# Performance work log

Hardware: AMD Instinct MI355X
Metric: run time of the kernel (lower is better)

The kernel has to match this reference:

```python
import jax, jax.numpy as jnp
import numpy as np

B, S, D, H = 4, 1024, 1024, 16
HD = D // H  # head dim = 64


def setup_inputs() -> dict:
    key = jax.random.key(0)
    ks = jax.random.split(key, 12)
    inv = 1.0 / np.sqrt(D)
    inp = {
        "q": jax.random.normal(ks[0], (B, S, D), jnp.float32),
        "k": jax.random.normal(ks[1], (B, S, D), jnp.float32),
        "v": jax.random.normal(ks[2], (B, S, D), jnp.float32),
        # additive-style mask: 1 where attention is disallowed (causal)
        "mask": jnp.triu(jnp.ones((S, S), jnp.float32), k=1)[None, None, :, :],
        "Wq": jax.random.normal(ks[3], (D, D), jnp.float32) * inv,
        "bq": jnp.zeros((D,), jnp.float32),
        "Wk": jax.random.normal(ks[4], (D, D), jnp.float32) * inv,
        "bk": jnp.zeros((D,), jnp.float32),
        "Wv": jax.random.normal(ks[5], (D, D), jnp.float32) * inv,
        "bv": jnp.zeros((D,), jnp.float32),
        "Wo": jax.random.normal(ks[6], (D, D), jnp.float32) * inv,
        "bo": jnp.zeros((D,), jnp.float32),
    }
    return inp


def _split_heads(x):
    # [b, s, (h d)] -> [b, h, s, d]
    b, s, _ = x.shape
    return x.reshape(b, s, H, HD).transpose(0, 2, 1, 3)


def reference(q, k, v, mask, Wq, bq, Wk, bk, Wv, bv, Wo, bo):
    query = _split_heads(q @ Wq + bq)   # [b,h,s,d]
    key = _split_heads(k @ Wk + bk)
    value = _split_heads(v @ Wv + bv)

    scores = jnp.einsum("bhqd,bhkd->bhqk", query, key) / np.sqrt(HD)
    scores = scores + mask * (-1e12)
    attention_weights = jax.nn.softmax(scores, axis=-1)  # [b,h,s,s]
    attn = jnp.einsum("bhqk,bhkd->bhqd", attention_weights, value)

    # dropout is identity in eval mode
    attn = attn.transpose(0, 2, 1, 3).reshape(q.shape[0], q.shape[1], D)
    out = attn @ Wo + bo
    return out, attention_weights
```

## Files before the change

### kernel.cpp

```cpp
#include <hip/hip_runtime.h>
#include <hip/hip_bf16.h>

#define B_ 4
#define S_ 1024
#define D_ 1024
#define H_ 16
#define HD_ 64
#define M_ (B_*S_)
#define NT_ (S_/64)

typedef __attribute__((ext_vector_type(8))) short bf16x8;
typedef __attribute__((ext_vector_type(8))) unsigned short u16x8;
typedef __attribute__((ext_vector_type(4))) float f32x4;

typedef __attribute__((address_space(1))) const unsigned int g_uint;
typedef __attribute__((address_space(3))) unsigned int l_uint;

__device__ __forceinline__ unsigned short f2bf(float f) {
  unsigned int x = __builtin_bit_cast(unsigned int, f);
  unsigned int r = (x + 0x7fffu + ((x >> 16) & 1u)) >> 16;
  return (unsigned short)r;
}
__device__ __forceinline__ float bf2f(unsigned short u) {
  unsigned int x = ((unsigned int)u) << 16;
  return __builtin_bit_cast(float, x);
}
__device__ __forceinline__ unsigned int cvtpk(float lo, float hi) {
  unsigned int r;
  asm("v_cvt_pk_bf16_f32 %0, %1, %2" : "=v"(r) : "v"(lo), "v"(hi));
  return r;
}
__device__ __forceinline__ void load_lds16(const ushort* g, ushort* l) {
  __builtin_amdgcn_global_load_lds((g_uint*)g, (l_uint*)l, 16, 0, 0);
}

__global__ void prep(const float* __restrict__ q, const float* __restrict__ k,
                     const float* __restrict__ v,
                     const float* __restrict__ Wq, const float* __restrict__ Wk,
                     const float* __restrict__ Wv, const float* __restrict__ Wo,
                     ushort* __restrict__ qo, ushort* __restrict__ ko, ushort* __restrict__ vo,
                     ushort* __restrict__ WqT, ushort* __restrict__ WkT,
                     ushort* __restrict__ WvT, ushort* __restrict__ WoT) {
  __shared__ float tile[32][33];
  int z = blockIdx.y;
  if (z < 3) {
    const float* s; ushort* d;
    switch (z) {
      case 0: s = q; d = qo; break;
      case 1: s = k; d = ko; break;
      default: s = v; d = vo; break;
    }
    int n4 = (M_ * D_) / 4;
    for (int i = blockIdx.x * blockDim.x + threadIdx.x; i < n4; i += gridDim.x * blockDim.x) {
      float4 x = reinterpret_cast<const float4*>(s)[i];
      ushort4 o;
      o.x = f2bf(x.x); o.y = f2bf(x.y); o.z = f2bf(x.z); o.w = f2bf(x.w);
      reinterpret_cast<ushort4*>(d)[i] = o;
    }
  } else {
    if (blockIdx.x >= 1024) return;
    const float* W; ushort* WT;
    switch (z - 3) {
      case 0: W = Wq; WT = WqT; break;
      case 1: W = Wk; WT = WkT; break;
      case 2: W = Wv; WT = WvT; break;
      default: W = Wo; WT = WoT; break;
    }
    int tx = threadIdx.x & 31, ty = threadIdx.x >> 5;
    int bx = (blockIdx.x & 31) * 32, by = (blockIdx.x >> 5) * 32;
    for (int r = 0; r < 32; r += 8)
      tile[ty + r][tx] = W[(size_t)(by + ty + r) * D_ + bx + tx];
    __syncthreads();
    for (int r = 0; r < 32; r += 8)
      WT[(size_t)(bx + ty + r) * D_ + by + tx] = f2bf(tile[tx][ty + r]);
  }
}

template <int BF16OUT, int BM, int BN>
__device__ __forceinline__ void gemm_body(const ushort* __restrict__ A,
                                          const ushort* __restrict__ Bt,
                                          const float* __restrict__ bias,
                                          void* __restrict__ Cp,
                                          int bm, int bn, int N, int K) {
  __shared__ ushort Al[BM * 64];
  __shared__ ushort Bl[BN * 64];
  constexpr int MF = BM / 32;
  constexpr int NF = BN / 32;
  const int tid = threadIdx.x;
  const int wave = tid >> 6, lane = tid & 63;
  const int r0 = lane & 15, kq = lane >> 4;
  const int wr = wave >> 1, wc = wave & 1;
  const int sl = lane >> 3;
  const int sc8 = ((lane & 7) ^ sl) * 8;
  f32x4 zero = {0.f, 0.f, 0.f, 0.f};
  f32x4 acc[MF][NF];
#pragma unroll
  for (int m = 0; m < MF; ++m)
#pragma unroll
    for (int n = 0; n < NF; ++n) acc[m][n] = zero;

  for (int kt = 0; kt < K; kt += 64) {
    __syncthreads();
#pragma unroll
    for (int i = 0; i < MF; ++i) {
      int c = wave * MF + i;
      load_lds16(A + (size_t)(bm + c * 8 + sl) * K + kt + sc8, &Al[c * 512]);
    }
#pragma unroll
    for (int i = 0; i < NF; ++i) {
      int c = wave * NF + i;
      load_lds16(Bt + (size_t)(bn + c * 8 + sl) * K + kt + sc8, &Bl[c * 512]);
    }
    __syncthreads();
#pragma unroll
    for (int kk = 0; kk < 2; ++kk) {
      bf16x8 a[MF], b[NF];
#pragma unroll
      for (int m = 0; m < MF; ++m)
        a[m] = *(const bf16x8*)&Al[(wr * (BM / 2) + m * 16 + r0) * 64 + (((kk * 4 + kq) ^ (r0 & 7)) * 8)];
#pragma unroll
      for (int n = 0; n < NF; ++n)
        b[n] = *(const bf16x8*)&Bl[(wc * (BN / 2) + n * 16 + r0) * 64 + (((kk * 4 + kq) ^ (r0 & 7)) * 8)];
#pragma unroll
      for (int m = 0; m < MF; ++m)
#pragma unroll
        for (int n = 0; n < NF; ++n)
          acc[m][n] = __builtin_amdgcn_mfma_f32_16x16x32_bf16(a[m], b[n], acc[m][n], 0, 0, 0);
    }
  }

#pragma unroll
  for (int m = 0; m < MF; ++m) {
#pragma unroll
    for (int n = 0; n < NF; ++n) {
      int col = bn + wc * (BN / 2) + n * 16 + r0;
      float bv = bias[col];
#pragma unroll
      for (int j = 0; j < 4; ++j) {
        int row = bm + wr * (BM / 2) + m * 16 + kq * 4 + j;
        float v = acc[m][n][j] + bv;
        if (BF16OUT) ((ushort*)Cp)[(size_t)row * N + col] = f2bf(v);
        else         ((float*)Cp)[(size_t)row * N + col] = v;
      }
    }
  }
}

__global__ __launch_bounds__(256) void gemm_qkv(const ushort* __restrict__ qa,
                                                const ushort* __restrict__ ka,
                                                const ushort* __restrict__ va,
                                                const ushort* __restrict__ WqT,
                                                const ushort* __restrict__ WkT,
                                                const ushort* __restrict__ WvT,
                                                const float* __restrict__ bq,
                                                const float* __restrict__ bk,
                                                const float* __restrict__ bv,
                                                ushort* __restrict__ Qo,
                                                ushort* __restrict__ Ko,
                                                ushort* __restrict__ Vo) {
  const ushort* A; const ushort* Bt; const float* bias; ushort* C;
  switch (blockIdx.z) {
    case 0: A = qa; Bt = WqT; bias = bq; C = Qo; break;
    case 1: A = ka; Bt = WkT; bias = bk; C = Ko; break;
    default: A = va; Bt = WvT; bias = bv; C = Vo; break;
  }
  gemm_body<1, 64, 128>(A, Bt, bias, C, blockIdx.x * 64, blockIdx.y * 128, D_, D_);
}

__global__ __launch_bounds__(256) void gemm_out(const ushort* __restrict__ A,
                                                const ushort* __restrict__ Bt,
                                                const float* __restrict__ bias,
                                                float* __restrict__ C) {
  gemm_body<0, 64, 128>(A, Bt, bias, C, blockIdx.x * 64, blockIdx.y * 128, D_, D_);
}

__global__ __launch_bounds__(256) void attn_fused(const ushort* __restrict__ Qb,
                                                  const ushort* __restrict__ Kb,
                                                  const ushort* __restrict__ Vb,
                                                  float* __restrict__ wout,
                                                  ushort* __restrict__ ctx) {
  const int id = blockIdx.x;
  const int bh = id & 63;
  const int b = bh >> 4, h = bh & 15;
  const int qt = NT_ - 1 - (id >> 6);
  const int tid = threadIdx.x, wave = tid >> 6, lane = tid & 63;
  const int r0 = lane & 15, kq = lane >> 4;
  const int sl = lane >> 3;
  const int sc8 = ((lane & 7) ^ sl) * 8;
  __shared__ ushort Kt[2][64 * 64];
  __shared__ ushort Vt[2][64 * 64];
  __shared__ ushort Wl[4][16 * 64];
  const size_t bh_off = ((size_t)(b * S_)) * D_ + (size_t)h * 64;
  float* wbase = wout + (size_t)bh * S_ * S_;
  const float KSC = 0.18033688011f;

  const ushort* Qg = Qb + bh_off + (size_t)(qt * 64 + wave * 16 + r0) * D_ + kq * 8;
  bf16x8 qa0 = *(const bf16x8*)Qg;
  bf16x8 qa1 = *(const bf16x8*)(Qg + 32);
  const int qglob = qt * 64 + wave * 16 + r0;

  auto stage_K = [&](int buf, int vb) {
    const ushort* Kg = Kb + bh_off + (size_t)(vb * 64) * D_;
#pragma unroll
    for (int i = 0; i < 2; ++i) {
      int c = wave * 2 + i;
      load_lds16(Kg + (size_t)(c * 8 + sl) * D_ + sc8, &Kt[buf][c * 512]);
    }
  };

  int cur = 0;
  stage_K(0, 0);
  float p0 = 0.f, p1 = 0.f, p2 = 0.f, p3 = 0.f;
  for (int vb = 0; vb <= qt; ++vb) {
    asm volatile("s_waitcnt vmcnt(0)" ::: "memory");
    __builtin_amdgcn_s_barrier();
    if (vb < qt) stage_K(cur ^ 1, vb + 1);
    const bool diag = (vb == qt);
#pragma unroll
    for (int jt = 0; jt < 4; ++jt) {
      int krow = jt * 16 + r0;
      bf16x8 kb0 = *(const bf16x8*)&Kt[cur][krow * 64 + ((kq ^ (r0 & 7)) * 8)];
      bf16x8 kb1 = *(const bf16x8*)&Kt[cur][krow * 64 + (((4 + kq) ^ (r0 & 7)) * 8)];
      f32x4 sc = {0.f, 0.f, 0.f, 0.f};
      sc = __builtin_amdgcn_mfma_f32_16x16x32_bf16(kb0, qa0, sc, 0, 0, 0);
      sc = __builtin_amdgcn_mfma_f32_16x16x32_bf16(kb1, qa1, sc, 0, 0, 0);
      int k0 = vb * 64 + jt * 16 + kq * 4;
      p0 += (diag && k0 + 0 > qglob) ? 0.f : exp2f(sc[0] * KSC);
      p1 += (diag && k0 + 1 > qglob) ? 0.f : exp2f(sc[1] * KSC);
      p2 += (diag && k0 + 2 > qglob) ? 0.f : exp2f(sc[2] * KSC);
      p3 += (diag && k0 + 3 > qglob) ? 0.f : exp2f(sc[3] * KSC);
    }
    cur ^= 1;
  }
  float ssum = (p0 + p1) + (p2 + p3);
  ssum += __shfl_xor(ssum, 16, 64);
  ssum += __shfl_xor(ssum, 32, 64);
  const float rs = 1.f / ssum;

  f32x4 zero = {0.f, 0.f, 0.f, 0.f};
  f32x4 cacc[4];
#pragma unroll
  for (int nt = 0; nt < 4; ++nt) cacc[nt] = zero;

  __syncthreads();
  uint4 vr[2];
  auto vload = [&](int vb) {
    const ushort* Vg = Vb + bh_off + (size_t)(vb * 64) * D_;
    vr[0] = *(const uint4*)&Vg[(size_t)lane * D_ + (size_t)(wave * 2 + 0) * 8];
    vr[1] = *(const uint4*)&Vg[(size_t)lane * D_ + (size_t)(wave * 2 + 1) * 8];
  };
  auto vwrite = [&](int buf) {
#pragma unroll
    for (int it = 0; it < 2; ++it) {
      int seg = wave * 2 + it;
      ushort tmp[8];
      *(uint4*)tmp = vr[it];
#pragma unroll
      for (int e = 0; e < 8; ++e) Vt[buf][(seg * 8 + e) * 64 + (lane ^ (e << 3))] = tmp[e];
    }
  };
  cur = 0;
  stage_K(0, 0);
  vload(0);
  vwrite(0);
  for (int vb = 0; vb <= qt; ++vb) {
    if (vb == 0) asm volatile("s_waitcnt vmcnt(0) lgkmcnt(0)" ::: "memory");
    else         asm volatile("s_waitcnt vmcnt(4) lgkmcnt(0)" ::: "memory");
    __builtin_amdgcn_s_barrier();
    if (vb < qt) { stage_K(cur ^ 1, vb + 1); vload(vb + 1); }
    const bool diag = (vb == qt);
#pragma unroll
    for (int jt = 0; jt < 4; ++jt) {
      int krow = jt * 16 + r0;
      bf16x8 kb0 = *(const bf16x8*)&Kt[cur][krow * 64 + ((kq ^ (r0 & 7)) * 8)];
      bf16x8 kb1 = *(const bf16x8*)&Kt[cur][krow * 64 + (((4 + kq) ^ (r0 & 7)) * 8)];
      f32x4 sc = {0.f, 0.f, 0.f, 0.f};
      sc = __builtin_amdgcn_mfma_f32_16x16x32_bf16(kb0, qa0, sc, 0, 0, 0);
      sc = __builtin_amdgcn_mfma_f32_16x16x32_bf16(kb1, qa1, sc, 0, 0, 0);
      int k0 = vb * 64 + jt * 16 + kq * 4;
      float e0 = (diag && k0 + 0 > qglob) ? 0.f : exp2f(sc[0] * KSC);
      float e1 = (diag && k0 + 1 > qglob) ? 0.f : exp2f(sc[1] * KSC);
      float e2 = (diag && k0 + 2 > qglob) ? 0.f : exp2f(sc[2] * KSC);
      float e3 = (diag && k0 + 3 > qglob) ? 0.f : exp2f(sc[3] * KSC);
      uint2 pk;
      pk.x = cvtpk(e0, e1);
      pk.y = cvtpk(e2, e3);
      int s = (4 * jt + kq) ^ ((r0 & 3) << 2);
      *(uint2*)&Wl[wave][r0 * 64 + s * 4] = pk;
      f32x4 o = {e0 * rs, e1 * rs, e2 * rs, e3 * rs};
      *(f32x4*)&wbase[(size_t)qglob * S_ + k0] = o;
    }
#pragma unroll
    for (int ks = 0; ks < 2; ++ks) {
      int sB = (8 * ks + 2 * kq) ^ ((r0 & 3) << 2);
      bf16x8 af = *(const bf16x8*)&Wl[wave][r0 * 64 + sB * 4];
#pragma unroll
      for (int nt = 0; nt < 4; ++nt) {
        bf16x8 vf = *(const bf16x8*)&Vt[cur][(nt * 16 + r0) * 64 + (((ks * 4 + kq) ^ (r0 & 7)) * 8)];
        cacc[nt] = __builtin_amdgcn_mfma_f32_16x16x32_bf16(af, vf, cacc[nt], 0, 0, 0);
      }
    }
    if (vb < qt) vwrite(cur ^ 1);
    cur ^= 1;
  }

  {
    int col0 = (qt + 1) * 64;
    int nf4 = (S_ - col0) >> 2;
    int row = tid >> 2, c = tid & 3;
    f32x4 z4 = {0.f, 0.f, 0.f, 0.f};
    float* rp = &wbase[(size_t)(qt * 64 + row) * S_];
    for (int i = c; i < nf4; i += 4) *(f32x4*)&rp[col0 + i * 4] = z4;
  }

  {
    float rsj[4];
#pragma unroll
    for (int j = 0; j < 4; ++j) rsj[j] = __shfl(rs, kq * 4 + j, 64);
    ushort* cg = ctx + ((size_t)(b * S_ + qt * 64 + wave * 16 + kq * 4)) * D_ + h * 64;
#pragma unroll
    for (int nt = 0; nt < 4; ++nt)
#pragma unroll
      for (int j = 0; j < 4; ++j)
        cg[(size_t)j * D_ + nt * 16 + r0] = f2bf(cacc[nt][j] * rsj[j]);
  }
}

extern "C" void kernel_launch(void* const* d_in, const int* in_sizes, int n_in,
                              void* d_out, int out_size, void* d_ws, size_t ws_size,
                              hipStream_t stream) {
  const float* q    = (const float*)d_in[0];
  const float* k    = (const float*)d_in[1];
  const float* v    = (const float*)d_in[2];
  const float* Wq   = (const float*)d_in[4];
  const float* bq   = (const float*)d_in[5];
  const float* Wk   = (const float*)d_in[6];
  const float* bk   = (const float*)d_in[7];
  const float* Wv   = (const float*)d_in[8];
  const float* bv   = (const float*)d_in[9];
  const float* Wo   = (const float*)d_in[10];
  const float* bo   = (const float*)d_in[11];

  char* ws = (char*)d_ws;
  const size_t MB = 1024 * 1024;
  ushort* q_bf   = (ushort*)(ws + 0 * MB);
  ushort* k_bf   = (ushort*)(ws + 8 * MB);
  ushort* v_bf   = (ushort*)(ws + 16 * MB);
  ushort* WqT    = (ushort*)(ws + 24 * MB);
  ushort* WkT    = (ushort*)(ws + 26 * MB);
  ushort* WvT    = (ushort*)(ws + 28 * MB);
  ushort* WoT    = (ushort*)(ws + 30 * MB);
  ushort* Q_bf   = (ushort*)(ws + 32 * MB);
  ushort* K_bf   = (ushort*)(ws + 40 * MB);
  ushort* V_bf   = (ushort*)(ws + 48 * MB);
  ushort* ctx_bf = (ushort*)(ws + 56 * MB);

  float* out  = (float*)d_out;
  float* wout = out + (size_t)M_ * D_;

  prep<<<dim3(2048, 7), 256, 0, stream>>>(q, k, v, Wq, Wk, Wv, Wo,
                                          q_bf, k_bf, v_bf, WqT, WkT, WvT, WoT);
  gemm_qkv<<<dim3(M_ / 64, D_ / 128, 3), 256, 0, stream>>>(
      q_bf, k_bf, v_bf, WqT, WkT, WvT, bq, bk, bv, Q_bf, K_bf, V_bf);
  attn_fused<<<dim3(1024), 256, 0, stream>>>(Q_bf, K_bf, V_bf, wout, ctx_bf);
  gemm_out<<<dim3(M_ / 64, D_ / 128), 256, 0, stream>>>(ctx_bf, WoT, bo, out);
}
```

Before: 165.4 us.

## Pair causal query tiles per block to balance attention work and shrink out-GEMM tile

Each attention block now handles two query tiles, the long tile qtA and the short tile qtB = 15-qtA, so every block does roughly equal causal work. The grid drops from 1024 to 512 blocks. The row-sum pass for tile B is folded into tile A's second pass, reusing the K tiles already in LDS. The output GEMM switches to 64x64 tiles with twice as many blocks, to fill more CUs. In exchange, each block runs longer with more registers live, and only 512 attention blocks are available to spread across CUs.

```diff
diff --git a/kernel.cpp b/kernel.cpp
--- a/kernel.cpp
+++ b/kernel.cpp
@@ -171,7 +171,7 @@
                                                 const ushort* __restrict__ Bt,
                                                 const float* __restrict__ bias,
                                                 float* __restrict__ C) {
-  gemm_body<0, 64, 128>(A, Bt, bias, C, blockIdx.x * 64, blockIdx.y * 128, D_, D_);
+  gemm_body<0, 64, 64>(A, Bt, bias, C, blockIdx.x * 64, blockIdx.y * 64, D_, D_);
 }
 
 __global__ __launch_bounds__(256) void attn_fused(const ushort* __restrict__ Qb,
@@ -182,7 +182,9 @@
   const int id = blockIdx.x;
   const int bh = id & 63;
   const int b = bh >> 4, h = bh & 15;
-  const int qt = NT_ - 1 - (id >> 6);
+  const int p = id >> 6;
+  const int qtA = NT_ - 1 - p;
+  const int qtB = p;
   const int tid = threadIdx.x, wave = tid >> 6, lane = tid & 63;
   const int r0 = lane & 15, kq = lane >> 4;
   const int sl = lane >> 3;
@@ -194,10 +196,14 @@
   float* wbase = wout + (size_t)bh * S_ * S_;
   const float KSC = 0.18033688011f;
 
-  const ushort* Qg = Qb + bh_off + (size_t)(qt * 64 + wave * 16 + r0) * D_ + kq * 8;
-  bf16x8 qa0 = *(const bf16x8*)Qg;
-  bf16x8 qa1 = *(const bf16x8*)(Qg + 32);
-  const int qglob = qt * 64 + wave * 16 + r0;
+  const ushort* QgA = Qb + bh_off + (size_t)(qtA * 64 + wave * 16 + r0) * D_ + kq * 8;
+  bf16x8 qa0A = *(const bf16x8*)QgA;
+  bf16x8 qa1A = *(const bf16x8*)(QgA + 32);
+  const ushort* QgB = Qb + bh_off + (size_t)(qtB * 64 + wave * 16 + r0) * D_ + kq * 8;
+  bf16x8 qa0B = *(const bf16x8*)QgB;
+  bf16x8 qa1B = *(const bf16x8*)(QgB + 32);
+  const int qgA = qtA * 64 + wave * 16 + r0;
+  const int qgB = qtB * 64 + wave * 16 + r0;
 
   auto stage_K = [&](int buf, int vb) {
     const ushort* Kg = Kb + bh_off + (size_t)(vb * 64) * D_;
@@ -207,42 +213,6 @@
       load_lds16(Kg + (size_t)(c * 8 + sl) * D_ + sc8, &Kt[buf][c * 512]);
     }
   };
-
-  int cur = 0;
-  stage_K(0, 0);
-  float p0 = 0.f, p1 = 0.f, p2 = 0.f, p3 = 0.f;
-  for (int vb = 0; vb <= qt; ++vb) {
-    asm volatile("s_waitcnt vmcnt(0)" ::: "memory");
-    __builtin_amdgcn_s_barrier();
-    if (vb < qt) stage_K(cur ^ 1, vb + 1);
-    const bool diag = (vb == qt);
-#pragma unroll
-    for (int jt = 0; jt < 4; ++jt) {
-      int krow = jt * 16 + r0;
-      bf16x8 kb0 = *(const bf16x8*)&Kt[cur][krow * 64 + ((kq ^ (r0 & 7)) * 8)];
-      bf16x8 kb1 = *(const bf16x8*)&Kt[cur][krow * 64 + (((4 + kq) ^ (r0 & 7)) * 8)];
-      f32x4 sc = {0.f, 0.f, 0.f, 0.f};
-      sc = __builtin_amdgcn_mfma_f32_16x16x32_bf16(kb0, qa0, sc, 0, 0, 0);
-      sc = __builtin_amdgcn_mfma_f32_16x16x32_bf16(kb1, qa1, sc, 0, 0, 0);
-      int k0 = vb * 64 + jt * 16 + kq * 4;
-      p0 += (diag && k0 + 0 > qglob) ? 0.f : exp2f(sc[0] * KSC);
-      p1 += (diag && k0 + 1 > qglob) ? 0.f : exp2f(sc[1] * KSC);
-      p2 += (diag && k0 + 2 > qglob) ? 0.f : exp2f(sc[2] * KSC);
-      p3 += (diag && k0 + 3 > qglob) ? 0.f : exp2f(sc[3] * KSC);
-    }
-    cur ^= 1;
-  }
-  float ssum = (p0 + p1) + (p2 + p3);
-  ssum += __shfl_xor(ssum, 16, 64);
-  ssum += __shfl_xor(ssum, 32, 64);
-  const float rs = 1.f / ssum;
-
-  f32x4 zero = {0.f, 0.f, 0.f, 0.f};
-  f32x4 cacc[4];
-#pragma unroll
-  for (int nt = 0; nt < 4; ++nt) cacc[nt] = zero;
-
-  __syncthreads();
   uint4 vr[2];
   auto vload = [&](int vb) {
     const ushort* Vg = Vb + bh_off + (size_t)(vb * 64) * D_;
@@ -259,36 +229,85 @@
       for (int e = 0; e < 8; ++e) Vt[buf][(seg * 8 + e) * 64 + (lane ^ (e << 3))] = tmp[e];
     }
   };
-  cur = 0;
+
+  f32x4 zero = {0.f, 0.f, 0.f, 0.f};
+
+  int cur = 0;
   stage_K(0, 0);
-  vload(0);
-  vwrite(0);
-  for (int vb = 0; vb <= qt; ++vb) {
-    if (vb == 0) asm volatile("s_waitcnt vmcnt(0) lgkmcnt(0)" ::: "memory");
-    else         asm volatile("s_waitcnt vmcnt(4) lgkmcnt(0)" ::: "memory");
+  float pA0 = 0.f, pA1 = 0.f, pA2 = 0.f, pA3 = 0.f;
+  for (int vb = 0; vb <= qtA; ++vb) {
+    asm volatile("s_waitcnt vmcnt(0)" ::: "memory");
     __builtin_amdgcn_s_barrier();
-    if (vb < qt) { stage_K(cur ^ 1, vb + 1); vload(vb + 1); }
-    const bool diag = (vb == qt);
+    if (vb < qtA) stage_K(cur ^ 1, vb + 1);
+    const bool diag = (vb == qtA);
 #pragma unroll
     for (int jt = 0; jt < 4; ++jt) {
       int krow = jt * 16 + r0;
       bf16x8 kb0 = *(const bf16x8*)&Kt[cur][krow * 64 + ((kq ^ (r0 & 7)) * 8)];
       bf16x8 kb1 = *(const bf16x8*)&Kt[cur][krow * 64 + (((4 + kq) ^ (r0 & 7)) * 8)];
       f32x4 sc = {0.f, 0.f, 0.f, 0.f};
-      sc = __builtin_amdgcn_mfma_f32_16x16x32_bf16(kb0, qa0, sc, 0, 0, 0);
-      sc = __builtin_amdgcn_mfma_f32_16x16x32_bf16(kb1, qa1, sc, 0, 0, 0);
+      sc = __builtin_amdgcn_mfma_f32_16x16x32_bf16(kb0, qa0A, sc, 0, 0, 0);
+      sc = __builtin_amdgcn_mfma_f32_16x16x32_bf16(kb1, qa1A, sc, 0, 0, 0);
       int k0 = vb * 64 + jt * 16 + kq * 4;
-      float e0 = (diag && k0 + 0 > qglob) ? 0.f : exp2f(sc[0] * KSC);
-      float e1 = (diag && k0 + 1 > qglob) ? 0.f : exp2f(sc[1] * KSC);
-      float e2 = (diag && k0 + 2 > qglob) ? 0.f : exp2f(sc[2] * KSC);
-      float e3 = (diag && k0 + 3 > qglob) ? 0.f : exp2f(sc[3] * KSC);
+      pA0 += (diag && k0 + 0 > qgA) ? 0.f : exp2f(sc[0] * KSC);
+      pA1 += (diag && k0 + 1 > qgA) ? 0.f : exp2f(sc[1] * KSC);
+      pA2 += (diag && k0 + 2 > qgA) ? 0.f : exp2f(sc[2] * KSC);
+      pA3 += (diag && k0 + 3 > qgA) ? 0.f : exp2f(sc[3] * KSC);
+    }
+    cur ^= 1;
+  }
+  float ssumA = (pA0 + pA1) + (pA2 + pA3);
+  ssumA += __shfl_xor(ssumA, 16, 64);
+  ssumA += __shfl_xor(ssumA, 32, 64);
+  const float rsA = 1.f / ssumA;
+
+  f32x4 caccA[4];
+#pragma unroll
+  for (int nt = 0; nt < 4; ++nt) caccA[nt] = zero;
+  float pB0 = 0.f, pB1 = 0.f, pB2 = 0.f, pB3 = 0.f;
+
+  __syncthreads();
+  cur = 0;
+  stage_K(0, 0);
+  vload(0);
+  vwrite(0);
+  for (int vb = 0; vb <= qtA; ++vb) {
+    if (vb == 0) asm volatile("s_waitcnt vmcnt(0) lgkmcnt(0)" ::: "memory");
+    else         asm volatile("s_waitcnt vmcnt(4) lgkmcnt(0)" ::: "memory");
+    __builtin_amdgcn_s_barrier();
+    if (vb < qtA) { stage_K(cur ^ 1, vb + 1); vload(vb + 1); }
+    const bool diagA = (vb == qtA);
+    const bool doB = (vb <= qtB);
+    const bool diagB = (vb == qtB);
+#pragma unroll
+    for (int jt = 0; jt < 4; ++jt) {
+      int krow = jt * 16 + r0;
+      bf16x8 kb0 = *(const bf16x8*)&Kt[cur][krow * 64 + ((kq ^ (r0 & 7)) * 8)];
+      bf16x8 kb1 = *(const bf16x8*)&Kt[cur][krow * 64 + (((4 + kq) ^ (r0 & 7)) * 8)];
+      int k0 = vb * 64 + jt * 16 + kq * 4;
+      f32x4 sc = {0.f, 0.f, 0.f, 0.f};
+      sc = __builtin_amdgcn_mfma_f32_16x16x32_bf16(kb0, qa0A, sc, 0, 0, 0);
+      sc = __builtin_amdgcn_mfma_f32_16x16x32_bf16(kb1, qa1A, sc, 0, 0, 0);
+      float e0 = (diagA && k0 + 0 > qgA) ? 0.f : exp2f(sc[0] * KSC);
+      float e1 = (diagA && k0 + 1 > qgA) ? 0.f : exp2f(sc[1] * KSC);
+      float e2 = (diagA && k0 + 2 > qgA) ? 0.f : exp2f(sc[2] * KSC);
+      float e3 = (diagA && k0 + 3 > qgA) ? 0.f : exp2f(sc[3] * KSC);
       uint2 pk;
       pk.x = cvtpk(e0, e1);
       pk.y = cvtpk(e2, e3);
       int s = (4 * jt + kq) ^ ((r0 & 3) << 2);
       *(uint2*)&Wl[wave][r0 * 64 + s * 4] = pk;
-      f32x4 o = {e0 * rs, e1 * rs, e2 * rs, e3 * rs};
-      *(f32x4*)&wbase[(size_t)qglob * S_ + k0] = o;
+      f32x4 o = {e0 * rsA, e1 * rsA, e2 * rsA, e3 * rsA};
+      *(f32x4*)&wbase[(size_t)qgA * S_ + k0] = o;
+      if (doB) {
+        f32x4 sb = {0.f, 0.f, 0.f, 0.f};
+        sb = __builtin_amdgcn_mfma_f32_16x16x32_bf16(kb0, qa0B, sb, 0, 0, 0);
+        sb = __builtin_amdgcn_mfma_f32_16x16x32_bf16(kb1, qa1B, sb, 0, 0, 0);
+        pB0 += (diagB && k0 + 0 > qgB) ? 0.f : exp2f(sb[0] * KSC);
+        pB1 += (diagB && k0 + 1 > qgB) ? 0.f : exp2f(sb[1] * KSC);
+        pB2 += (diagB && k0 + 2 > qgB) ? 0.f : exp2f(sb[2] * KSC);
+        pB3 += (diagB && k0 + 3 > qgB) ? 0.f : exp2f(sb[3] * KSC);
+      }
     }
 #pragma unroll
     for (int ks = 0; ks < 2; ++ks) {
@@ -297,32 +316,104 @@
 #pragma unroll
       for (int nt = 0; nt < 4; ++nt) {
         bf16x8 vf = *(const bf16x8*)&Vt[cur][(nt * 16 + r0) * 64 + (((ks * 4 + kq) ^ (r0 & 7)) * 8)];
-        cacc[nt] = __builtin_amdgcn_mfma_f32_16x16x32_bf16(af, vf, cacc[nt], 0, 0, 0);
+        caccA[nt] = __builtin_amdgcn_mfma_f32_16x16x32_bf16(af, vf, caccA[nt], 0, 0, 0);
       }
     }
-    if (vb < qt) vwrite(cur ^ 1);
+    if (vb < qtA) vwrite(cur ^ 1);
     cur ^= 1;
   }
+  float ssumB = (pB0 + pB1) + (pB2 + pB3);
+  ssumB += __shfl_xor(ssumB, 16, 64);
+  ssumB += __shfl_xor(ssumB, 32, 64);
+  const float rsB = 1.f / ssumB;
 
   {
-    int col0 = (qt + 1) * 64;
+    int col0 = (qtA + 1) * 64;
     int nf4 = (S_ - col0) >> 2;
     int row = tid >> 2, c = tid & 3;
     f32x4 z4 = {0.f, 0.f, 0.f, 0.f};
-    float* rp = &wbase[(size_t)(qt * 64 + row) * S_];
+    float* rp = &wbase[(size_t)(qtA * 64 + row) * S_];
     for (int i = c; i < nf4; i += 4) *(f32x4*)&rp[col0 + i * 4] = z4;
   }
-
   {
     float rsj[4];
 #pragma unroll
-    for (int j = 0; j < 4; ++j) rsj[j] = __shfl(rs, kq * 4 + j, 64);
-    ushort* cg = ctx + ((size_t)(b * S_ + qt * 64 + wave * 16 + kq * 4)) * D_ + h * 64;
+    for (int j = 0; j < 4; ++j) rsj[j] = __shfl(rsA, kq * 4 + j, 64);
+    ushort* cg = ctx + ((size_t)(b * S_ + qtA * 64 + wave * 16 + kq * 4)) * D_ + h * 64;
 #pragma unroll
     for (int nt = 0; nt < 4; ++nt)
 #pragma unroll
       for (int j = 0; j < 4; ++j)
-        cg[(size_t)j * D_ + nt * 16 + r0] = f2bf(cacc[nt][j] * rsj[j]);
+        cg[(size_t)j * D_ + nt * 16 + r0] = f2bf(caccA[nt][j] * rsj[j]);
+  }
+
+  f32x4 caccB[4];
+#pragma unroll
+  for (int nt = 0; nt < 4; ++nt) caccB[nt] = zero;
+  __syncthreads();
+  cur = 0;
+  stage_K(0, 0);
+  vload(0);
+  vwrite(0);
+  for (int vb = 0; vb <= qtB; ++vb) {
+    if (vb == 0) asm volatile("s_waitcnt vmcnt(0) lgkmcnt(0)" ::: "memory");
+    else         asm volatile("s_waitcnt vmcnt(4) lgkmcnt(0)" ::: "memory");
+    __builtin_amdgcn_s_barrier();
+    if (vb < qtB) { stage_K(cur ^ 1, vb + 1); vload(vb + 1); }
+    const bool diag = (vb == qtB);
+#pragma unroll
+    for (int jt = 0; jt < 4; ++jt) {
+      int krow = jt * 16 + r0;
+      bf16x8 kb0 = *(const bf16x8*)&Kt[cur][krow * 64 + ((kq ^ (r0 & 7)) * 8)];
+      bf16x8 kb1 = *(const bf16x8*)&Kt[cur][krow * 64 + (((4 + kq) ^ (r0 & 7)) * 8)];
+      f32x4 sc = {0.f, 0.f, 0.f, 0.f};
+      sc = __builtin_amdgcn_mfma_f32_16x16x32_bf16(kb0, qa0B, sc, 0, 0, 0);
+      sc = __builtin_amdgcn_mfma_f32_16x16x32_bf16(kb1, qa1B, sc, 0, 0, 0);
+      int k0 = vb * 64 + jt * 16 + kq * 4;
+      float e0 = (diag && k0 + 0 > qgB) ? 0.f : exp2f(sc[0] * KSC);
+      float e1 = (diag && k0 + 1 > qgB) ? 0.f : exp2f(sc[1] * KSC);
+      float e2 = (diag && k0 + 2 > qgB) ? 0.f : exp2f(sc[2] * KSC);
+      float e3 = (diag && k0 + 3 > qgB) ? 0.f : exp2f(sc[3] * KSC);
+      uint2 pk;
+      pk.x = cvtpk(e0, e1);
+      pk.y = cvtpk(e2, e3);
+      int s = (4 * jt + kq) ^ ((r0 & 3) << 2);
+      *(uint2*)&Wl[wave][r0 * 64 + s * 4] = pk;
+      f32x4 o = {e0 * rsB, e1 * rsB, e2 * rsB, e3 * rsB};
+      *(f32x4*)&wbase[(size_t)qgB * S_ + k0] = o;
+    }
+#pragma unroll
+    for (int ks = 0; ks < 2; ++ks) {
+      int sB = (8 * ks + 2 * kq) ^ ((r0 & 3) << 2);
+      bf16x8 af = *(const bf16x8*)&Wl[wave][r0 * 64 + sB * 4];
+#pragma unroll
+      for (int nt = 0; nt < 4; ++nt) {
+        bf16x8 vf = *(const bf16x8*)&Vt[cur][(nt * 16 + r0) * 64 + (((ks * 4 + kq) ^ (r0 & 7)) * 8)];
+        caccB[nt] = __builtin_amdgcn_mfma_f32_16x16x32_bf16(af, vf, caccB[nt], 0, 0, 0);
+      }
+    }
+    if (vb < qtB) vwrite(cur ^ 1);
+    cur ^= 1;
+  }
+
+  {
+    int col0 = (qtB + 1) * 64;
+    int nf4 = (S_ - col0) >> 2;
+    int row = tid >> 2, c = tid & 3;
+    f32x4 z4 = {0.f, 0.f, 0.f, 0.f};
+    float* rp = &wbase[(size_t)(qtB * 64 + row) * S_];
+    for (int i = c; i < nf4; i += 4) *(f32x4*)&rp[col0 + i * 4] = z4;
+  }
+  {
+    float rsj[4];
+#pragma unroll
+    for (int j = 0; j < 4; ++j) rsj[j] = __shfl(rsB, kq * 4 + j, 64);
+    ushort* cg = ctx + ((size_t)(b * S_ + qtB * 64 + wave * 16 + kq * 4)) * D_ + h * 64;
+#pragma unroll
+    for (int nt = 0; nt < 4; ++nt)
+#pragma unroll
+      for (int j = 0; j < 4; ++j)
+        cg[(size_t)j * D_ + nt * 16 + r0] = f2bf(caccB[nt][j] * rsj[j]);
   }
 }
 
@@ -362,6 +453,6 @@
                                           q_bf, k_bf, v_bf, WqT, WkT, WvT, WoT);
   gemm_qkv<<<dim3(M_ / 64, D_ / 128, 3), 256, 0, stream>>>(
       q_bf, k_bf, v_bf, WqT, WkT, WvT, bq, bk, bv, Q_bf, K_bf, V_bf);
-  attn_fused<<<dim3(1024), 256, 0, stream>>>(Q_bf, K_bf, V_bf, wout, ctx_bf);
-  gemm_out<<<dim3(M_ / 64, D_ / 128), 256, 0, stream>>>(ctx_bf, WoT, bo, out);
-}
+  attn_fused<<<dim3(512), 256, 0, stream>>>(Q_bf, K_bf, V_bf, wout, ctx_bf);
+  gemm_out<<<dim3(M_ / 64, D_ / 64), 256, 0, stream>>>(ctx_bf, WoT, bo, out);
+}
```

After: 164.4 us. No clear change (-0.6%).
